# Kernel tuning notes

Hardware: AMD Instinct MI355X
Metric: run time of the kernel (lower is better)

## Reference

```python
import jax, jax.numpy as jnp
import numpy as np

K = 20  # neighbors
EPS = 1e-5

def lrelu(x):
    return jnp.where(x >= 0, x, 0.2 * x)

def knn_idx(x, k):
    # x: [B, C, N] -> idx [B, N, k] of nearest neighbors (includes self)
    xx = jnp.sum(x * x, axis=1)                      # [B, N]
    inner = jnp.einsum('bcn,bcm->bnm', x, x)         # [B, N, N]
    neg_dist = 2.0 * inner - xx[:, :, None] - xx[:, None, :]
    return jax.lax.top_k(neg_dist, k)[1]

def get_graph_feature(x, k):
    # x: [B, C, N] -> [B, 2C, N, k] = concat(neighbor - center, center)
    idx = knn_idx(x, k)                              # [B, N, k]
    xt = jnp.transpose(x, (0, 2, 1))                 # [B, N, C]
    nb = jax.vmap(lambda t, i: t[i])(xt, idx)        # [B, N, k, C]
    ctr = jnp.broadcast_to(xt[:, :, None, :], nb.shape)
    feat = jnp.concatenate([nb - ctr, ctr], axis=-1) # [B, N, k, 2C]
    return jnp.transpose(feat, (0, 3, 1, 2))

def conv_bn2d(x, W, g, b):
    # 1x1 Conv2d (no bias) + training-mode BN + LeakyReLU(0.2)
    y = jnp.einsum('oc,bcnk->bonk', W, x)
    m = jnp.mean(y, axis=(0, 2, 3), keepdims=True)
    v = jnp.var(y, axis=(0, 2, 3), keepdims=True)
    y = g.reshape(1, -1, 1, 1) * (y - m) * jax.lax.rsqrt(v + EPS) + b.reshape(1, -1, 1, 1)
    return lrelu(y)

def conv_bn1d(x, W, g, b):
    y = jnp.einsum('oc,bcn->bon', W, x)
    m = jnp.mean(y, axis=(0, 2), keepdims=True)
    v = jnp.var(y, axis=(0, 2), keepdims=True)
    y = g.reshape(1, -1, 1) * (y - m) * jax.lax.rsqrt(v + EPS) + b.reshape(1, -1, 1)
    return lrelu(y)

def bn_vec(y, g, b):
    m = jnp.mean(y, axis=0, keepdims=True)
    v = jnp.var(y, axis=0, keepdims=True)
    return g * (y - m) * jax.lax.rsqrt(v + EPS) + b

def setup_inputs() -> dict:
    key = jax.random.key(0)
    ks = jax.random.split(key, 16)
    s = 0.05
    d = {
        'x':  jax.random.normal(ks[0], (8, 3, 1024), dtype=jnp.float32),
        'W1': jax.random.normal(ks[1], (64, 6)) * s,
        'W2': jax.random.normal(ks[2], (64, 128)) * s,
        'W3': jax.random.normal(ks[3], (128, 128)) * s,
        'W4': jax.random.normal(ks[4], (256, 256)) * s,
        'W5': jax.random.normal(ks[5], (1024, 512)) * s,
        'Wl1': jax.random.normal(ks[6], (512, 2048)) * s,
        'Wl2': jax.random.normal(ks[7], (256, 512)) * s,
        'bl2': jnp.zeros((256,)),
        'Wl3': jax.random.normal(ks[8], (40, 256)) * s,
        'bl3': jnp.zeros((40,)),
    }
    for i, c in zip(range(1, 8), [64, 64, 128, 256, 1024, 512, 256]):
        d[f'g{i}'] = 1.0 + s * jax.random.normal(jax.random.fold_in(key, 100 + i), (c,))
        d[f'b{i}'] = s * jax.random.normal(jax.random.fold_in(key, 200 + i), (c,))
    return d

def reference(x, W1, W2, W3, W4, W5, Wl1, Wl2, bl2, Wl3, bl3,
              g1, b1, g2, b2, g3, b3, g4, b4, g5, b5, g6, b6, g7, b7):
    f = get_graph_feature(x, K)          # [B, 6, N, k]
    x1 = conv_bn2d(f, W1, g1, b1).max(axis=-1)   # [B, 64, N]
    f = get_graph_feature(x1, K)
    x2 = conv_bn2d(f, W2, g2, b2).max(axis=-1)   # [B, 64, N]
    f = get_graph_feature(x2, K)
    x3 = conv_bn2d(f, W3, g3, b3).max(axis=-1)   # [B, 128, N]
    f = get_graph_feature(x3, K)
    x4 = conv_bn2d(f, W4, g4, b4).max(axis=-1)   # [B, 256, N]
    h = jnp.concatenate([x1, x2, x3, x4], axis=1)  # [B, 512, N]
    h = conv_bn1d(h, W5, g5, b5)                   # [B, 1024, N]
    z = jnp.concatenate([h.max(axis=-1), h.mean(axis=-1)], axis=1)  # [B, 2048]
    z = lrelu(bn_vec(z @ Wl1.T, g6, b6))
    z = lrelu(bn_vec(z @ Wl2.T + bl2, g7, b7))
    return z @ Wl3.T + bl3
```

## Files before the change

kernel.cpp:

```cpp
#include <hip/hip_runtime.h>
#include <hip/hip_bf16.h>
#include <cstdint>


static constexpr int BB  = 8;
static constexpr int NN  = 1024;
static constexpr int KNB = 20;
static constexpr float BNEPS = 1e-5f;

static constexpr int NIN = 25;

__constant__ int c_cum[NIN + 1] = {
    0, 24576, 24960, 33152, 49536, 115072, 639360,
    1687936, 1819008, 1819264, 1829504, 1829544, 1829608, 1829672, 1829736,
    1829800, 1829928, 1830056, 1830312, 1830568, 1831592, 1832616, 1833128,
    1833640, 1833896, 1834152};
__constant__ int c_trO[NIN] = {0, 64, 64, 128, 256, 1024, 0, 0, 0, 0, 0,
                               0, 0, 0, 0, 0, 0, 0, 0, 0, 0, 0, 0, 0, 0};
__constant__ int c_trI[NIN] = {0, 6, 128, 128, 256, 512, 0, 0, 0, 0, 0,
                               0, 0, 0, 0, 0, 0, 0, 0, 0, 0, 0, 0, 0, 0};

enum : int {
  XIN = 0, WT1 = 24576, WT2 = 24960, WT3 = 33152, WT4 = 49536, WT5 = 115072,
  WL1 = 639360, WL2 = 1687936, BL2o = 1819008, WL3 = 1819264, BL3o = 1829504,
  G1 = 1829544, B1o = 1829608, G2 = 1829672, B2o = 1829736,
  G3 = 1829800, B3o = 1829928, G4 = 1830056, B4o = 1830312,
  G5 = 1830568, B5o = 1831592, G6 = 1832616, B6o = 1833128,
  G7 = 1833640, B7o = 1833896,
  IDXo = 1842432,
  HCATo = 2006272,
  STATSo = 6200576,
  Z2048o = 6237440,
  Z1o = 6253824,
  Z2o = 6257920,
  FLAGSo = 6259968,
  DISTo = 6260736,
  HBFo  = 14649344,
  W5BFo = 16746496
};
static constexpr int TOTAL_IN = 1834152;
static constexpr int NCONV = (TOTAL_IN + 255) / 256;
static constexpr int U_OFF   = DISTo + 0;
static constexpr int VD_OFF  = DISTo + 2097152;
static constexpr int YS_OFF  = DISTo + 4194304;
static constexpr int Y5_OFF  = DISTo + 0;
static constexpr size_t WS_NEED_MFMA = (size_t)17008640 * 4;

struct Ptrs { const void* p[NIN]; };

typedef short short8v __attribute__((ext_vector_type(8)));
typedef float f32x16 __attribute__((ext_vector_type(16)));

__device__ __forceinline__ float lrelu(float y) { return (y < 0.f) ? 0.2f * y : y; }
__device__ __forceinline__ unsigned short f2b(float f) {
  unsigned u = __float_as_uint(f);
  unsigned r = (u + 0x7FFFu + ((u >> 16) & 1u)) >> 16;
  return (unsigned short)r;
}
__device__ __forceinline__ unsigned f2s(float f) {
  const unsigned s = __float_as_uint(f);
  return s ^ ((unsigned)((int)s >> 31) | 0x80000000u);
}
__device__ __forceinline__ bool kbetter_u(unsigned v, int i, unsigned v2, int i2) {
  return v > v2 || (v == v2 && i < i2);
}
__device__ __forceinline__ float load_in(const void* p, int fl, int idx) {
  if (fl == 2) return 0.f;
  if (fl == 1) {
    const unsigned short u = ((const unsigned short*)p)[idx];
    return __uint_as_float(((unsigned)u) << 16);
  }
  return ((const float*)p)[idx];
}
__device__ __forceinline__ int mbcnt64(unsigned long long m) {
  return __builtin_amdgcn_mbcnt_hi((unsigned)(m >> 32),
                                   __builtin_amdgcn_mbcnt_lo((unsigned)m, 0));
}

__global__ void detect_kernel(Ptrs ptrs, int* __restrict__ flags) {
  const int i = blockIdx.x;
  const unsigned* p = (const unsigned*)ptrs.p[i];
  const int n = c_cum[i + 1] - c_cum[i];
  int words = n >> 1; if (words > 64) words = 64;
  const int t = threadIdx.x;
  unsigned w = (t < words) ? p[t] : 0u;
  bool nz = (w != 0u);
  unsigned e = (w >> 7) & 0xFFu;
  bool pl = nz && (e >= 96u) && (e <= 140u);
  unsigned long long mnz = __ballot(nz);
  unsigned long long mpl = __ballot(pl);
  if (t == 0) {
    int cnz = __popcll(mnz), cpl = __popcll(mpl);
    flags[i] = (cnz == 0) ? 2 : ((2 * cpl > words) ? 1 : 0);
  }
}

__global__ void convert_kernel(Ptrs ptrs, const int* __restrict__ flags,
                               float* __restrict__ ws, int do_w5) {
  const int bx = blockIdx.x;
  const int t = threadIdx.x;
  if (bx >= NCONV + 80) {
    if (!do_w5) return;
    const int g = (bx - NCONV - 80) * 256 + t;
    const int lane = g & 63;
    const int kb = (g >> 6) & 31;
    const int ot = g >> 11;
    const int o = ot * 32 + (lane & 31);
    const int k0 = kb * 16 + (lane >> 5) * 8;
    const void* w5raw = ptrs.p[5];
    const int fl = flags[5];
    unsigned u[4];
#pragma unroll
    for (int h = 0; h < 4; ++h) {
      const unsigned short lo = f2b(load_in(w5raw, fl, o * 512 + k0 + 2 * h));
      const unsigned short hi = f2b(load_in(w5raw, fl, o * 512 + k0 + 2 * h + 1));
      u[h] = (unsigned)lo | ((unsigned)hi << 16);
    }
    unsigned short* w5p = (unsigned short*)(ws + W5BFo);
    *(uint4*)&w5p[(size_t)g * 8] = make_uint4(u[0], u[1], u[2], u[3]);
    return;
  }
  if (bx >= NCONV) {
    const int z = (bx - NCONV) * 256 + t;
    if (z < 20480) ws[STATSo + z] = 0.f;
    return;
  }
  const int e = bx * 256 + t;
  if (e >= TOTAL_IN) return;
  int i = 0;
  while (e >= c_cum[i + 1]) ++i;
  if (do_w5 && i == 5) return;
  const int el = e - c_cum[i];
  int src;
  const int O = c_trO[i];
  if (O > 0) {
    const int I = c_trI[i];
    const int o = el % O, ii = el / O;
    src = o * I + ii;
  } else src = el;
  ws[e] = load_in(ptrs.p[i], flags[i], src);
}

template <int C>
__global__ __launch_bounds__(256) void dist2_kernel(
    const float* __restrict__ xbase, int bstr, float* __restrict__ D) {
  __shared__ __align__(16) float s_a[16][128];
  __shared__ __align__(16) float s_b[16][128];
  __shared__ float s_xx[256];
  const int t = threadIdx.x;
  const int bx = blockIdx.x;
  const int b = bx >> 6;
  const int r = bx & 63;
  const int tn0 = (r >> 3) * 128;
  const int tm0 = (r & 7) * 128;
  const float* xb = xbase + (size_t)b * bstr;
  {
    const int idx = (t < 128) ? (tn0 + t) : (tm0 + (t - 128));
    float s = 0.f;
    for (int c = 0; c < C; ++c) {
      const float v = xb[c * NN + idx];
      s = fmaf(v, v, s);
    }
    s_xx[t] = s;
  }
  const int tn = (t >> 4) * 8;
  const int tm = (t & 15) * 8;
  float acc[8][8] = {};
  for (int c0 = 0; c0 < C; c0 += 16) {
    const int kc = (C - c0 < 16) ? (C - c0) : 16;
    __syncthreads();
    for (int i = t; i < 512; i += 256) {
      const int cc = i >> 5, col4 = (i & 31) * 4;
      float4 va = make_float4(0.f, 0.f, 0.f, 0.f), vb = va;
      if (cc < kc) {
        va = *(const float4*)&xb[(c0 + cc) * NN + tn0 + col4];
        vb = *(const float4*)&xb[(c0 + cc) * NN + tm0 + col4];
      }
      *(float4*)&s_a[cc][col4] = va;
      *(float4*)&s_b[cc][col4] = vb;
    }
    __syncthreads();
#pragma unroll
    for (int cc = 0; cc < 16; ++cc) {
      const float4 a0 = *(const float4*)&s_a[cc][tn];
      const float4 a1 = *(const float4*)&s_a[cc][tn + 4];
      const float4 b0 = *(const float4*)&s_b[cc][tm];
      const float4 b1 = *(const float4*)&s_b[cc][tm + 4];
      const float aa[8] = {a0.x, a0.y, a0.z, a0.w, a1.x, a1.y, a1.z, a1.w};
      const float bb2[8] = {b0.x, b0.y, b0.z, b0.w, b1.x, b1.y, b1.z, b1.w};
#pragma unroll
      for (int i = 0; i < 8; ++i)
#pragma unroll
        for (int j = 0; j < 8; ++j) acc[i][j] = fmaf(aa[i], bb2[j], acc[i][j]);
    }
  }
  float xmv[8];
#pragma unroll
  for (int j = 0; j < 8; ++j) xmv[j] = s_xx[128 + tm + j];
  float* Db = D + ((size_t)b << 20);
#pragma unroll
  for (int i = 0; i < 8; ++i) {
    const float xxn = s_xx[tn + i];
    float4 o0v, o1v;
    o0v.x = 2.f * acc[i][0] - xxn - xmv[0];
    o0v.y = 2.f * acc[i][1] - xxn - xmv[1];
    o0v.z = 2.f * acc[i][2] - xxn - xmv[2];
    o0v.w = 2.f * acc[i][3] - xxn - xmv[3];
    o1v.x = 2.f * acc[i][4] - xxn - xmv[4];
    o1v.y = 2.f * acc[i][5] - xxn - xmv[5];
    o1v.z = 2.f * acc[i][6] - xxn - xmv[6];
    o1v.w = 2.f * acc[i][7] - xxn - xmv[7];
    float* row = &Db[(size_t)(tn0 + tn + i) * NN + tm0 + tm];
    *(float4*)row = o0v;
    *(float4*)(row + 4) = o1v;
  }
}

__device__ __forceinline__ void tk_ins_u(unsigned v, int i, unsigned ku[4],
                                         int ki[4]) {
  if (kbetter_u(v, i, ku[3], ki[3])) {
    ku[3] = v; ki[3] = i;
    if (kbetter_u(ku[3], ki[3], ku[2], ki[2])) {
      unsigned tv = ku[2]; int ti = ki[2];
      ku[2] = ku[3]; ki[2] = ki[3]; ku[3] = tv; ki[3] = ti;
    }
    if (kbetter_u(ku[2], ki[2], ku[1], ki[1])) {
      unsigned tv = ku[1]; int ti = ki[1];
      ku[1] = ku[2]; ki[1] = ki[2]; ku[2] = tv; ki[2] = ti;
    }
    if (kbetter_u(ku[1], ki[1], ku[0], ki[0])) {
      unsigned tv = ku[0]; int ti = ki[0];
      ku[0] = ku[1]; ki[0] = ki[1]; ku[1] = tv; ki[1] = ti;
    }
  }
}

__device__ __forceinline__ void tk_build_u(const float* __restrict__ Dr,
                                           int base, unsigned mask,
                                           unsigned ku[4], int ki[4]) {
#pragma unroll
  for (int q = 0; q < 4; ++q) { ku[q] = 0u; ki[q] = 0x7FFFFFFF; }
  const float4 a0 = *(const float4*)&Dr[base + 0];
  const float4 a1 = *(const float4*)&Dr[base + 4];
  const float4 a2 = *(const float4*)&Dr[base + 8];
  const float4 a3 = *(const float4*)&Dr[base + 12];
  const float vs[16] = {a0.x, a0.y, a0.z, a0.w, a1.x, a1.y, a1.z, a1.w,
                        a2.x, a2.y, a2.z, a2.w, a3.x, a3.y, a3.z, a3.w};
#pragma unroll
  for (int j = 0; j < 16; ++j)
    if (!((mask >> j) & 1u)) tk_ins_u(f2s(vs[j]), base + j, ku, ki);
}

template <int C, int O>
__global__ __launch_bounds__(256) void tg_kernel(
    const float* __restrict__ D, int* __restrict__ idxb,
    const float* __restrict__ xbase, int bstr, const float* __restrict__ WT,
    float* __restrict__ U, float* __restrict__ Vd) {
  constexpr int OT = O / 64;
  __shared__ __align__(16) float s_pool[1536];
  const int t = threadIdx.x;
  if (blockIdx.x < 2048) {
    const int lane = t & 63;
    const int wv = t >> 6;
    const int row = blockIdx.x * 4 + wv;
    const float* Dr = D + ((size_t)row << 10);
    const int base = lane * 16;
    const float4 a0 = *(const float4*)&Dr[base + 0];
    const float4 a1 = *(const float4*)&Dr[base + 4];
    const float4 a2 = *(const float4*)&Dr[base + 8];
    const float4 a3 = *(const float4*)&Dr[base + 12];
    unsigned k[16] = {f2s(a0.x), f2s(a0.y), f2s(a0.z), f2s(a0.w),
                      f2s(a1.x), f2s(a1.y), f2s(a1.z), f2s(a1.w),
                      f2s(a2.x), f2s(a2.y), f2s(a2.z), f2s(a2.w),
                      f2s(a3.x), f2s(a3.y), f2s(a3.z), f2s(a3.w)};
    unsigned lmax = 0u;
#pragma unroll
    for (int j = 0; j < 16; ++j) lmax = (k[j] > lmax) ? k[j] : lmax;
    unsigned T = 0u;
    for (int b = 31; b >= 0; --b) {
      const unsigned cand = T | (1u << b);
      if (__popcll(__ballot(lmax >= cand)) >= KNB) T = cand;
    }
    int cnt = 0;
#pragma unroll
    for (int j = 0; j < 16; ++j) cnt += (k[j] >= T) ? 1 : 0;
    int n_c = 0, off = 0;
#pragma unroll
    for (int b = 0; b < 5; ++b) {
      const unsigned long long m = __ballot((cnt >> b) & 1);
      n_c += __popcll(m) << b;
      off += mbcnt64(m) << b;
    }
    unsigned long long* sc = (unsigned long long*)s_pool + wv * 128;
    if (n_c <= 128) {
#pragma unroll
      for (int j = 0; j < 16; ++j)
        if (k[j] >= T) {
          sc[off] = (((unsigned long long)k[j]) << 32) |
                    (unsigned long long)(0xFFFFFFFFu ^ (unsigned)(base + j));
          ++off;
        }
      if (n_c <= 64) {
        unsigned long long mye = 0ULL;
        if (lane < n_c) mye = sc[lane];
        int rank = 0;
        for (int j = 0; j < n_c; ++j) {
          const unsigned eh =
              (unsigned)__builtin_amdgcn_readlane((int)(mye >> 32), j);
          const unsigned el =
              (unsigned)__builtin_amdgcn_readlane((int)(mye & 0xFFFFFFFFu), j);
          const unsigned long long ej = (((unsigned long long)eh) << 32) | el;
          rank += (ej > mye) ? 1 : 0;
        }
        if (lane < n_c && rank < KNB)
          idxb[row * KNB + rank] =
              (int)(0xFFFFFFFFu ^ (unsigned)(mye & 0xFFFFFFFFu));
      } else {
        const unsigned long long mye = (lane < n_c) ? sc[lane] : 0ULL;
        const unsigned long long mye2 = (64 + lane < n_c) ? sc[64 + lane] : 0ULL;
        int r1 = 0, r2 = 0;
        for (int j = 0; j < n_c; ++j) {
          const unsigned long long ej = sc[j];
          r1 += (ej > mye) ? 1 : 0;
          r2 += (ej > mye2) ? 1 : 0;
        }
        if (lane < n_c && r1 < KNB)
          idxb[row * KNB + r1] = (int)(0xFFFFFFFFu ^ (unsigned)mye);
        if (64 + lane < n_c && r2 < KNB)
          idxb[row * KNB + r2] = (int)(0xFFFFFFFFu ^ (unsigned)mye2);
      }
      return;
    }
    unsigned ku[4]; int ki[4];
    tk_build_u(Dr, base, 0u, ku, ki);
    unsigned maskex = 0;
    for (int kk = 0; kk < KNB; ++kk) {
      unsigned bv = ku[0];
#pragma unroll
      for (int off2 = 1; off2 < 64; off2 <<= 1) {
        const unsigned pv = (unsigned)__shfl_xor((int)bv, off2, 64);
        bv = (pv > bv) ? pv : bv;
      }
      const unsigned long long m = __ballot(ku[0] == bv);
      const int wl = __ffsll(m) - 1;
      const int bi = __shfl(ki[0], wl, 64);
      if (lane == 0) idxb[row * KNB + kk] = bi;
      if (lane == wl) {
        maskex |= 1u << (bi & 15);
        ku[0] = ku[1]; ki[0] = ki[1];
        ku[1] = ku[2]; ki[1] = ki[2];
        ku[2] = ku[3]; ki[2] = ki[3];
        ku[3] = 0u; ki[3] = 0x7FFFFFFF;
        if (ki[0] == 0x7FFFFFFF && __popc(maskex) < 16)
          tk_build_u(Dr, base, maskex, ku, ki);
      }
    }
    return;
  }
  float (*s_x)[64] = (float(*)[64])(s_pool);
  float (*s_wn)[64] = (float(*)[64])(s_pool + 512);
  float (*s_wc)[64] = (float(*)[64])(s_pool + 1024);
  const int bx = blockIdx.x - 2048;
  const int b = bx / (16 * OT);
  const int r = bx % (16 * OT);
  const int n0 = (r / OT) * 64;
  const int o0 = (r % OT) * 64;
  const float* xb = xbase + (size_t)b * bstr;
  const int tn = (t >> 4) * 4;
  const int to = (t & 15) * 4;
  float accU[4][4] = {}, accC[4][4] = {};
  for (int c0 = 0; c0 < C; c0 += 8) {
    const int kc = (C - c0 < 8) ? (C - c0) : 8;
    for (int i = t; i < 8 * 64; i += 256) {
      const int cc = i >> 6, col = i & 63;
      const bool ok = cc < kc;
      s_x[cc][col]  = ok ? xb[(c0 + cc) * NN + n0 + col] : 0.f;
      s_wn[cc][col] = ok ? WT[(c0 + cc) * O + o0 + col] : 0.f;
      s_wc[cc][col] = ok ? WT[(C + c0 + cc) * O + o0 + col] : 0.f;
    }
    __syncthreads();
#pragma unroll
    for (int cc = 0; cc < 8; ++cc) {
      const float4 xv = *(const float4*)&s_x[cc][tn];
      const float4 wn = *(const float4*)&s_wn[cc][to];
      const float4 wc = *(const float4*)&s_wc[cc][to];
      const float xa[4] = {xv.x, xv.y, xv.z, xv.w};
      const float na[4] = {wn.x, wn.y, wn.z, wn.w};
      const float ca[4] = {wc.x, wc.y, wc.z, wc.w};
#pragma unroll
      for (int i = 0; i < 4; ++i)
#pragma unroll
        for (int j = 0; j < 4; ++j) {
          accU[i][j] = fmaf(xa[i], na[j], accU[i][j]);
          accC[i][j] = fmaf(xa[i], ca[j], accC[i][j]);
        }
    }
    __syncthreads();
  }
#pragma unroll
  for (int i = 0; i < 4; ++i) {
    const size_t base2 = ((size_t)(b << 10) + n0 + tn + i) * O + o0 + to;
    *(float4*)&U[base2] = make_float4(accU[i][0], accU[i][1], accU[i][2], accU[i][3]);
    *(float4*)&Vd[base2] = make_float4(accC[i][0] - accU[i][0], accC[i][1] - accU[i][1],
                                       accC[i][2] - accU[i][2], accC[i][3] - accU[i][3]);
  }
}

template <int O>
__global__ __launch_bounds__(256) void edge_pass_kernel(
    const float* __restrict__ U, const float* __restrict__ Vd,
    const int* __restrict__ idxb, const float* __restrict__ g,
    float* __restrict__ stats, float* __restrict__ ysel) {
  constexpr int PSUB = 256 / O;
  __shared__ float s_red[256];
  const int t = threadIdx.x;
  const int o = t & (O - 1);
  const int psub = t / O;
  const bool usemax = g[o] >= 0.f;
  float ls1 = 0.f, ls2 = 0.f;
  for (int p = blockIdx.x * PSUB + psub; p < BB * NN; p += gridDim.x * PSUB) {
    const int b = p >> 10;
    const float* ub = U + ((size_t)(b << 10)) * O;
    int id[KNB];
#pragma unroll
    for (int k = 0; k < KNB; ++k) id[k] = idxb[p * KNB + k];
    const float vd = Vd[(size_t)p * O + o];
    float ymx = -3.4e38f, ymn = 3.4e38f;
#pragma unroll
    for (int k = 0; k < KNB; ++k) {
      const float y = ub[(size_t)id[k] * O + o] + vd;
      ymx = fmaxf(ymx, y);
      ymn = fminf(ymn, y);
      ls1 += y;
      ls2 = fmaf(y, y, ls2);
    }
    ysel[(size_t)p * O + o] = usemax ? ymx : ymn;
  }
  if (PSUB == 1) {
    atomicAdd(&stats[o], ls1);
    atomicAdd(&stats[1024 + o], ls2);
  } else {
    s_red[t] = ls1;
    __syncthreads();
    if (t < O) {
      float s = s_red[t];
#pragma unroll
      for (int p2 = 1; p2 < PSUB; ++p2) s += s_red[t + p2 * O];
      atomicAdd(&stats[t], s);
    }
    __syncthreads();
    s_red[t] = ls2;
    __syncthreads();
    if (t < O) {
      float s = s_red[t];
#pragma unroll
      for (int p2 = 1; p2 < PSUB; ++p2) s += s_red[t + p2 * O];
      atomicAdd(&stats[1024 + t], s);
    }
  }
}

template <int O>
__global__ __launch_bounds__(256) void bn_apply_kernel(
    const float* __restrict__ ysel, const float* __restrict__ stats,
    const float* __restrict__ g, const float* __restrict__ bb,
    float* __restrict__ hout, unsigned short* __restrict__ hp, int coff) {
  constexpr int OT = O / 32;
  __shared__ float s_t[32][33];
  const int t = threadIdx.x;
  const int bx = blockIdx.x;
  const int b = bx / (32 * OT);
  const int r = bx % (32 * OT);
  const int n0 = (r / OT) * 32;
  const int o0 = (r % OT) * 32;
  const int col = t & 31, rowb = t >> 5;
  const int o = o0 + col;
  const float inv = 1.f / (8.f * 1024.f * 20.f);
  const float mean = stats[o] * inv;
  const float var = stats[1024 + o] * inv - mean * mean;
  const float sc = g[o] * rsqrtf(var + BNEPS);
  const float sh = bb[o] - mean * sc;
  const int c = coff + o;
#pragma unroll
  for (int rr = 0; rr < 4; ++rr) {
    const int nl = n0 + rowb + rr * 8;
    const float y = ysel[((size_t)(b << 10) + nl) * O + o];
    const float h = lrelu(fmaf(sc, y, sh));
    if (hout) s_t[rowb + rr * 8][col] = h;
    if (hp) {
      const int lane2 = (nl & 31) + ((c >> 3) & 1) * 32;
      hp[(((size_t)(b * 32 + (nl >> 5)) * 32 + (c >> 4)) * 64 + lane2) * 8 +
         (c & 7)] = f2b(h);
    }
  }
  if (hout) {
    __syncthreads();
#pragma unroll
    for (int rr = 0; rr < 4; ++rr) {
      const int ol = rowb + rr * 8;
      hout[(size_t)b * (512 * 1024) + (o0 + ol) * NN + n0 + col] = s_t[col][ol];
    }
  }
}

__global__ __launch_bounds__(256) void conv1d_mfma_kernel(
    const unsigned short* __restrict__ hp,
    const unsigned short* __restrict__ w5p, float* __restrict__ Y5) {
  const int t = threadIdx.x, bx = blockIdx.x;
  const int b = bx >> 6;
  const int r = bx & 63;
  const int w = t >> 6, lane = t & 63;
  const int ot0 = (r >> 3) * 4 + (w & 1) * 2;
  const int nt0 = (r & 7) * 4 + (w >> 1) * 2;
  const unsigned short* a0p = w5p + (size_t)ot0 * 16384 + lane * 8;
  const unsigned short* a1p = a0p + 16384;
  const unsigned short* b0p = hp + (size_t)(b * 32 + nt0) * 16384 + lane * 8;
  const unsigned short* b1p = b0p + 16384;
  f32x16 acc00, acc01, acc10, acc11;
#pragma unroll
  for (int i = 0; i < 16; ++i) { acc00[i] = 0.f; acc01[i] = 0.f; acc10[i] = 0.f; acc11[i] = 0.f; }
#pragma unroll 2
  for (int kb = 0; kb < 32; ++kb) {
    const int off = kb * 512;
    const short8v a0 = *(const short8v*)(a0p + off);
    const short8v a1 = *(const short8v*)(a1p + off);
    const short8v b0 = *(const short8v*)(b0p + off);
    const short8v b1 = *(const short8v*)(b1p + off);
    acc00 = __builtin_amdgcn_mfma_f32_32x32x16_bf16(a0, b0, acc00, 0, 0, 0);
    acc01 = __builtin_amdgcn_mfma_f32_32x32x16_bf16(a0, b1, acc01, 0, 0, 0);
    acc10 = __builtin_amdgcn_mfma_f32_32x32x16_bf16(a1, b0, acc10, 0, 0, 0);
    acc11 = __builtin_amdgcn_mfma_f32_32x32x16_bf16(a1, b1, acc11, 0, 0, 0);
  }
  const int l31 = lane & 31, l5 = lane >> 5;
#pragma unroll
  for (int oi = 0; oi < 2; ++oi) {
#pragma unroll
    for (int nj = 0; nj < 2; ++nj) {
      const f32x16 a = (oi == 0) ? (nj == 0 ? acc00 : acc01)
                                 : (nj == 0 ? acc10 : acc11);
      const int ob = (ot0 + oi) * 32;
      const int nb = (nt0 + nj) * 32;
#pragma unroll
      for (int r16 = 0; r16 < 16; ++r16) {
        const int row = (r16 & 3) + 8 * (r16 >> 2) + 4 * l5;
        Y5[((size_t)(b << 10) + ob + row) * 1024 + nb + l31] = a[r16];
      }
    }
  }
}

__global__ __launch_bounds__(256) void c1pool_kernel(
    const float* __restrict__ Y5, const float* __restrict__ g,
    const float* __restrict__ bb, float* __restrict__ z) {
  __shared__ __align__(16) float s_y[8][1024];
  __shared__ float sr[256];
  __shared__ float s_par[2];
  const int o = blockIdx.x, t = threadIdx.x;
  float s1 = 0.f, s2 = 0.f;
#pragma unroll
  for (int b = 0; b < 8; ++b) {
    const float4 v = *(const float4*)&Y5[((size_t)((b << 10) + o)) * 1024 + t * 4];
    *(float4*)&s_y[b][t * 4] = v;
    s1 += v.x + v.y + v.z + v.w;
    s2 = fmaf(v.x, v.x, s2);
    s2 = fmaf(v.y, v.y, s2);
    s2 = fmaf(v.z, v.z, s2);
    s2 = fmaf(v.w, v.w, s2);
  }
  sr[t] = s1;
  __syncthreads();
  for (int s = 128; s > 0; s >>= 1) {
    if (t < s) sr[t] += sr[t + s];
    __syncthreads();
  }
  if (t == 0) s_par[0] = sr[0];
  __syncthreads();
  sr[t] = s2;
  __syncthreads();
  for (int s = 128; s > 0; s >>= 1) {
    if (t < s) sr[t] += sr[t + s];
    __syncthreads();
  }
  if (t == 0) {
    const float mean = s_par[0] * (1.f / 8192.f);
    const float var = sr[0] * (1.f / 8192.f) - mean * mean;
    const float sc = g[o] * rsqrtf(var + BNEPS);
    s_par[0] = sc;
    s_par[1] = bb[o] - mean * sc;
  }
  __syncthreads();
  const float sc = s_par[0], sh = s_par[1];
  const int lane = t & 63, w = t >> 6;
#pragma unroll
  for (int h = 0; h < 2; ++h) {
    const int b = w + h * 4;
    float mx = -3.4e38f, sm = 0.f;
#pragma unroll
    for (int j = 0; j < 4; ++j) {
      const float4 v = *(const float4*)&s_y[b][lane * 16 + j * 4];
      const float y0 = lrelu(fmaf(sc, v.x, sh));
      const float y1 = lrelu(fmaf(sc, v.y, sh));
      const float y2 = lrelu(fmaf(sc, v.z, sh));
      const float y3 = lrelu(fmaf(sc, v.w, sh));
      mx = fmaxf(fmaxf(fmaxf(mx, y0), fmaxf(y1, y2)), y3);
      sm += y0 + y1 + y2 + y3;
    }
#pragma unroll
    for (int off = 1; off < 64; off <<= 1) {
      mx = fmaxf(mx, __shfl_xor(mx, off, 64));
      sm += __shfl_xor(sm, off, 64);
    }
    if (lane == 0) {
      z[b * 2048 + o] = mx;
      z[b * 2048 + 1024 + o] = sm * (1.f / 1024.f);
    }
  }
}

__global__ void bn_finalize_kernel(float* __restrict__ stats,
                                   const float* __restrict__ g,
                                   const float* __restrict__ bb, int cout,
                                   float inv_cnt) {
  const int o = blockIdx.x * 256 + threadIdx.x;
  if (o >= cout) return;
  const float mean = stats[o] * inv_cnt;
  const float var = stats[1024 + o] * inv_cnt - mean * mean;
  const float s = g[o] * rsqrtf(var + BNEPS);
  stats[2048 + o] = s;
  stats[3072 + o] = bb[o] - mean * s;
}

__global__ __launch_bounds__(256) void conv1d_gemm_kernel(
    const float* __restrict__ hcat, const float* __restrict__ WT5,
    float* __restrict__ stats, float* __restrict__ Y5) {
  __shared__ __align__(16) float s_w[8][64];
  __shared__ __align__(16) float s_h[8][64];
  __shared__ __align__(16) float s_red[64][16];
  const int t = threadIdx.x;
  const int bx = blockIdx.x;
  const int b = bx >> 8;
  const int o0 = ((bx >> 4) & 15) * 64;
  const int n0 = (bx & 15) * 64;
  const float* hb = hcat + (size_t)b * (512 * 1024);
  const int to = (t >> 4) * 4;
  const int tn = (t & 15) * 4;
  float acc[4][4] = {};
  for (int c0 = 0; c0 < 512; c0 += 8) {
    for (int i = t; i < 8 * 64; i += 256) {
      const int cc = i >> 6, col = i & 63;
      s_w[cc][col] = WT5[(c0 + cc) * 1024 + o0 + col];
      s_h[cc][col] = hb[(c0 + cc) * NN + n0 + col];
    }
    __syncthreads();
#pragma unroll
    for (int cc = 0; cc < 8; ++cc) {
      const float4 wv = *(const float4*)&s_w[cc][to];
      const float4 hv = *(const float4*)&s_h[cc][tn];
      const float wa[4] = {wv.x, wv.y, wv.z, wv.w};
      const float ha[4] = {hv.x, hv.y, hv.z, hv.w};
#pragma unroll
      for (int i = 0; i < 4; ++i)
#pragma unroll
        for (int j = 0; j < 4; ++j) acc[i][j] = fmaf(wa[i], ha[j], acc[i][j]);
    }
    __syncthreads();
  }
#pragma unroll
  for (int i = 0; i < 4; ++i) {
    *(float4*)&Y5[((size_t)(b << 10) + o0 + to + i) * NN + n0 + tn] =
        make_float4(acc[i][0], acc[i][1], acc[i][2], acc[i][3]);
  }
#pragma unroll
  for (int i = 0; i < 4; ++i)
    s_red[to + i][t & 15] = acc[i][0] + acc[i][1] + acc[i][2] + acc[i][3];
  __syncthreads();
  if (t < 64) {
    float s = 0.f;
#pragma unroll
    for (int g2 = 0; g2 < 16; ++g2) s += s_red[t][g2];
    atomicAdd(&stats[o0 + t], s);
  }
  __syncthreads();
#pragma unroll
  for (int i = 0; i < 4; ++i) {
    float s = 0.f;
#pragma unroll
    for (int j = 0; j < 4; ++j) s = fmaf(acc[i][j], acc[i][j], s);
    s_red[to + i][t & 15] = s;
  }
  __syncthreads();
  if (t < 64) {
    float s = 0.f;
#pragma unroll
    for (int g2 = 0; g2 < 16; ++g2) s += s_red[t][g2];
    atomicAdd(&stats[1024 + o0 + t], s);
  }
}

__global__ __launch_bounds__(256) void pool_kernel(
    const float* __restrict__ Y5, const float* __restrict__ stats,
    float* __restrict__ z) {
  const int t = threadIdx.x;
  const int lane = t & 63;
  const int bx = blockIdx.x;
  const int b = bx >> 8;
  const int o = (bx & 255) * 4 + (t >> 6);
  const float sc = stats[2048 + o], sh = stats[3072 + o];
  const float* yr = Y5 + ((size_t)(b << 10) + o) * NN;
  float mx = -3.4e38f, sm = 0.f;
#pragma unroll
  for (int j = 0; j < 16; ++j) {
    const float y = lrelu(fmaf(sc, yr[j * 64 + lane], sh));
    mx = fmaxf(mx, y);
    sm += y;
  }
  for (int off = 32; off > 0; off >>= 1) {
    mx = fmaxf(mx, __shfl_down(mx, off, 64));
    sm += __shfl_down(sm, off, 64);
  }
  if (lane == 0) {
    z[b * 2048 + o] = mx;
    z[b * 2048 + 1024 + o] = sm * (1.f / 1024.f);
  }
}

__global__ __launch_bounds__(256) void mlp_kernel(
    const float* __restrict__ zin, const float* __restrict__ W,
    const float* __restrict__ bias, const float* __restrict__ g,
    const float* __restrict__ bb, int kin, float* __restrict__ out, int O) {
  __shared__ float s_red[256];
  __shared__ float s_y[8];
  const int t = threadIdx.x;
  const int o = blockIdx.x;
  float acc[8];
#pragma unroll
  for (int b = 0; b < 8; ++b) acc[b] = 0.f;
  for (int c = t; c < kin; c += 256) {
    const float w = W[(size_t)o * kin + c];
#pragma unroll
    for (int b = 0; b < 8; ++b) acc[b] = fmaf(w, zin[b * kin + c], acc[b]);
  }
  for (int b = 0; b < 8; ++b) {
    s_red[t] = acc[b];
    __syncthreads();
    for (int s = 128; s > 0; s >>= 1) {
      if (t < s) s_red[t] += s_red[t + s];
      __syncthreads();
    }
    if (t == 0) s_y[b] = s_red[0] + (bias ? bias[o] : 0.f);
    __syncthreads();
  }
  if (t == 0) {
    float m = 0.f;
    for (int b = 0; b < 8; ++b) m += s_y[b];
    m *= 0.125f;
    float v = 0.f;
    for (int b = 0; b < 8; ++b) { const float d = s_y[b] - m; v = fmaf(d, d, v); }
    v *= 0.125f;
    const float s = g[o] * rsqrtf(v + BNEPS);
    const float sh = bb[o] - m * s;
    for (int b = 0; b < 8; ++b) out[b * O + o] = lrelu(fmaf(s, s_y[b], sh));
  }
}

__global__ void final_kernel(const float* __restrict__ z2,
                             const float* __restrict__ Wl3,
                             const float* __restrict__ bl3,
                             const int* __restrict__ flags, void* out) {
  const int j = blockIdx.x * 256 + threadIdx.x;
  if (j >= 320) return;
  int anyf32 = 0, anybf = 0;
  for (int i = 0; i < NIN; ++i) {
    const int fl = flags[i];
    if (fl == 0) anyf32 = 1;
    if (fl == 1) anybf = 1;
  }
  const int bf16out = (anybf && !anyf32) ? 1 : 0;
  const int b = j / 40, o = j - b * 40;
  float s = bl3[o];
  for (int c = 0; c < 256; ++c) s = fmaf(z2[b * 256 + c], Wl3[o * 256 + c], s);
  if (bf16out) ((__hip_bfloat16*)out)[j] = __float2bfloat16(s);
  else ((float*)out)[j] = s;
}

template <int C, int O>
static void run_stage(float* wsf, const float* xbase, int bstr, int widx,
                      int gidx, int bidx, int stat, float* hout,
                      unsigned short* hp, int coff, hipStream_t stream) {
  int* idxb = reinterpret_cast<int*>(wsf + IDXo);
  float* dist = wsf + DISTo;
  float* U = wsf + U_OFF;
  float* Vd = wsf + VD_OFF;
  float* ysel = wsf + YS_OFF;
  float* stats = wsf + STATSo + stat * 4096;
  dist2_kernel<C><<<512, 256, 0, stream>>>(xbase, bstr, dist);
  tg_kernel<C, O><<<2048 + BB * 16 * (O / 64), 256, 0, stream>>>(
      dist, idxb, xbase, bstr, wsf + widx, U, Vd);
  edge_pass_kernel<O><<<512, 256, 0, stream>>>(U, Vd, idxb, wsf + gidx, stats,
                                               ysel);
  bn_apply_kernel<O><<<BB * 32 * (O / 32), 256, 0, stream>>>(
      ysel, stats, wsf + gidx, wsf + bidx, hout, hp, coff);
}

extern "C" void kernel_launch(void* const* d_in, const int* in_sizes, int n_in,
                              void* d_out, int out_size, void* d_ws,
                              size_t ws_size, hipStream_t stream) {
  (void)in_sizes; (void)n_in; (void)out_size;
  float* wsf = reinterpret_cast<float*>(d_ws);
  int* flags = reinterpret_cast<int*>(wsf + FLAGSo);
  float* hcat = wsf + HCATo;
  const bool mf = ws_size >= WS_NEED_MFMA;
  unsigned short* hp = mf ? reinterpret_cast<unsigned short*>(wsf + HBFo) : nullptr;
  unsigned short* w5p = reinterpret_cast<unsigned short*>(wsf + W5BFo);

  Ptrs ptrs;
  for (int i = 0; i < NIN; ++i) ptrs.p[i] = d_in[i];

  detect_kernel<<<NIN, 64, 0, stream>>>(ptrs, flags);
  convert_kernel<<<NCONV + 80 + 256, 256, 0, stream>>>(ptrs, flags, wsf,
                                                       mf ? 1 : 0);

  run_stage<3, 64>(wsf, wsf + XIN, 3 * NN, WT1, G1, B1o, 0, hcat, hp, 0,
                   stream);
  run_stage<64, 64>(wsf, hcat, 512 * NN, WT2, G2, B2o, 1, hcat + 64 * NN, hp,
                    64, stream);
  run_stage<64, 128>(wsf, hcat + 64 * NN, 512 * NN, WT3, G3, B3o, 2,
                     hcat + 128 * NN, hp, 128, stream);
  run_stage<128, 256>(wsf, hcat + 128 * NN, 512 * NN, WT4, G4, B4o, 3,
                      mf ? nullptr : (hcat + 256 * NN), hp, 256, stream);

  float* Y5 = wsf + Y5_OFF;
  float* st5 = wsf + STATSo + 4 * 4096;
  if (mf) {
    conv1d_mfma_kernel<<<512, 256, 0, stream>>>(hp, w5p, Y5);
    c1pool_kernel<<<1024, 256, 0, stream>>>(Y5, wsf + G5, wsf + B5o,
                                            wsf + Z2048o);
  } else {
    conv1d_gemm_kernel<<<2048, 256, 0, stream>>>(hcat, wsf + WT5, st5, Y5);
    bn_finalize_kernel<<<4, 256, 0, stream>>>(st5, wsf + G5, wsf + B5o, 1024,
                                              1.f / 8192.f);
    pool_kernel<<<BB * 256, 256, 0, stream>>>(Y5, st5, wsf + Z2048o);
  }

  mlp_kernel<<<512, 256, 0, stream>>>(wsf + Z2048o, wsf + WL1, nullptr,
      wsf + G6, wsf + B6o, 2048, wsf + Z1o, 512);
  mlp_kernel<<<256, 256, 0, stream>>>(wsf + Z1o, wsf + WL2, wsf + BL2o,
      wsf + G7, wsf + B7o, 512, wsf + Z2o, 256);
  final_kernel<<<2, 256, 0, stream>>>(wsf + Z2o, wsf + WL3, wsf + BL3o,
      flags, d_out);
}
```

Measured before the change: 470.5 us.

## Skip converting MLP weights; read raw inputs directly in MLP kernels

When the MFMA path is active, the convert kernel now only processes the small leading inputs and the BN parameter tail, skipping the large Wl1/Wl2/Wl3 copies into workspace. The MLP and final kernels instead read the original input buffers through the dtype-aware loader using the detected flags. The edge_pass kernel grid is also raised from 512 to 2048 blocks to add parallelism. The direct reads add a per-element flag branch in the MLP loops. The larger edge_pass grid assumes the kernel handles the extra blocks correctly.

```diff
diff --git a/kernel.cpp b/kernel.cpp
--- a/kernel.cpp
+++ b/kernel.cpp
@@ -40,6 +40,8 @@
 };
 static constexpr int TOTAL_IN = 1834152;
 static constexpr int NCONV = (TOTAL_IN + 255) / 256;
+static constexpr int NMAIN_ELEMS = 115072 + 4608;
+static constexpr int NMAIN_MF = (NMAIN_ELEMS + 255) / 256;
 static constexpr int U_OFF   = DISTo + 0;
 static constexpr int VD_OFF  = DISTo + 2097152;
 static constexpr int YS_OFF  = DISTo + 4194304;
@@ -96,12 +98,12 @@
 }
 
 __global__ void convert_kernel(Ptrs ptrs, const int* __restrict__ flags,
-                               float* __restrict__ ws, int do_w5) {
+                               float* __restrict__ ws, int do_w5, int nmain) {
   const int bx = blockIdx.x;
   const int t = threadIdx.x;
-  if (bx >= NCONV + 80) {
+  if (bx >= nmain + 80) {
     if (!do_w5) return;
-    const int g = (bx - NCONV - 80) * 256 + t;
+    const int g = (bx - nmain - 80) * 256 + t;
     const int lane = g & 63;
     const int kb = (g >> 6) & 31;
     const int ot = g >> 11;
@@ -120,16 +122,22 @@
     *(uint4*)&w5p[(size_t)g * 8] = make_uint4(u[0], u[1], u[2], u[3]);
     return;
   }
-  if (bx >= NCONV) {
-    const int z = (bx - NCONV) * 256 + t;
+  if (bx >= nmain) {
+    const int z = (bx - nmain) * 256 + t;
     if (z < 20480) ws[STATSo + z] = 0.f;
     return;
   }
-  const int e = bx * 256 + t;
-  if (e >= TOTAL_IN) return;
+  int e;
+  if (do_w5) {
+    const int e2 = bx * 256 + t;
+    if (e2 >= NMAIN_ELEMS) return;
+    e = (e2 < 115072) ? e2 : (e2 - 115072 + 1829544);
+  } else {
+    e = bx * 256 + t;
+    if (e >= TOTAL_IN) return;
+  }
   int i = 0;
   while (e >= c_cum[i + 1]) ++i;
-  if (do_w5 && i == 5) return;
   const int el = e - c_cum[i];
   int src;
   const int O = c_trO[i];
@@ -725,18 +733,20 @@
 }
 
 __global__ __launch_bounds__(256) void mlp_kernel(
-    const float* __restrict__ zin, const float* __restrict__ W,
-    const float* __restrict__ bias, const float* __restrict__ g,
-    const float* __restrict__ bb, int kin, float* __restrict__ out, int O) {
+    const float* __restrict__ zin, const void* __restrict__ W,
+    const void* __restrict__ bias, const int* __restrict__ flags, int wfl,
+    int bfl, const float* __restrict__ g, const float* __restrict__ bb,
+    int kin, float* __restrict__ out, int O) {
   __shared__ float s_red[256];
   __shared__ float s_y[8];
   const int t = threadIdx.x;
   const int o = blockIdx.x;
+  const int fw = flags[wfl];
   float acc[8];
 #pragma unroll
   for (int b = 0; b < 8; ++b) acc[b] = 0.f;
   for (int c = t; c < kin; c += 256) {
-    const float w = W[(size_t)o * kin + c];
+    const float w = load_in(W, fw, o * kin + c);
 #pragma unroll
     for (int b = 0; b < 8; ++b) acc[b] = fmaf(w, zin[b * kin + c], acc[b]);
   }
@@ -747,7 +757,8 @@
       if (t < s) s_red[t] += s_red[t + s];
       __syncthreads();
     }
-    if (t == 0) s_y[b] = s_red[0] + (bias ? bias[o] : 0.f);
+    if (t == 0)
+      s_y[b] = s_red[0] + (bias ? load_in(bias, flags[bfl], o) : 0.f);
     __syncthreads();
   }
   if (t == 0) {
@@ -764,8 +775,8 @@
 }
 
 __global__ void final_kernel(const float* __restrict__ z2,
-                             const float* __restrict__ Wl3,
-                             const float* __restrict__ bl3,
+                             const void* __restrict__ Wl3,
+                             const void* __restrict__ bl3,
                              const int* __restrict__ flags, void* out) {
   const int j = blockIdx.x * 256 + threadIdx.x;
   if (j >= 320) return;
@@ -776,9 +787,11 @@
     if (fl == 1) anybf = 1;
   }
   const int bf16out = (anybf && !anyf32) ? 1 : 0;
+  const int fw = flags[9], fb = flags[10];
   const int b = j / 40, o = j - b * 40;
-  float s = bl3[o];
-  for (int c = 0; c < 256; ++c) s = fmaf(z2[b * 256 + c], Wl3[o * 256 + c], s);
+  float s = load_in(bl3, fb, o);
+  for (int c = 0; c < 256; ++c)
+    s = fmaf(z2[b * 256 + c], load_in(Wl3, fw, o * 256 + c), s);
   if (bf16out) ((__hip_bfloat16*)out)[j] = __float2bfloat16(s);
   else ((float*)out)[j] = s;
 }
@@ -796,8 +809,8 @@
   dist2_kernel<C><<<512, 256, 0, stream>>>(xbase, bstr, dist);
   tg_kernel<C, O><<<2048 + BB * 16 * (O / 64), 256, 0, stream>>>(
       dist, idxb, xbase, bstr, wsf + widx, U, Vd);
-  edge_pass_kernel<O><<<512, 256, 0, stream>>>(U, Vd, idxb, wsf + gidx, stats,
-                                               ysel);
+  edge_pass_kernel<O><<<2048, 256, 0, stream>>>(U, Vd, idxb, wsf + gidx,
+                                                stats, ysel);
   bn_apply_kernel<O><<<BB * 32 * (O / 32), 256, 0, stream>>>(
       ysel, stats, wsf + gidx, wsf + bidx, hout, hp, coff);
 }
@@ -817,8 +830,9 @@
   for (int i = 0; i < NIN; ++i) ptrs.p[i] = d_in[i];
 
   detect_kernel<<<NIN, 64, 0, stream>>>(ptrs, flags);
-  convert_kernel<<<NCONV + 80 + 256, 256, 0, stream>>>(ptrs, flags, wsf,
-                                                       mf ? 1 : 0);
+  const int nmain = mf ? NMAIN_MF : NCONV;
+  convert_kernel<<<nmain + 80 + 256, 256, 0, stream>>>(ptrs, flags, wsf,
+                                                       mf ? 1 : 0, nmain);
 
   run_stage<3, 64>(wsf, wsf + XIN, 3 * NN, WT1, G1, B1o, 0, hcat, hp, 0,
                    stream);
@@ -842,10 +856,10 @@
     pool_kernel<<<BB * 256, 256, 0, stream>>>(Y5, st5, wsf + Z2048o);
   }
 
-  mlp_kernel<<<512, 256, 0, stream>>>(wsf + Z2048o, wsf + WL1, nullptr,
-      wsf + G6, wsf + B6o, 2048, wsf + Z1o, 512);
-  mlp_kernel<<<256, 256, 0, stream>>>(wsf + Z1o, wsf + WL2, wsf + BL2o,
-      wsf + G7, wsf + B7o, 512, wsf + Z2o, 256);
-  final_kernel<<<2, 256, 0, stream>>>(wsf + Z2o, wsf + WL3, wsf + BL3o,
+  mlp_kernel<<<512, 256, 0, stream>>>(wsf + Z2048o, d_in[6], nullptr, flags,
+      6, 0, wsf + G6, wsf + B6o, 2048, wsf + Z1o, 512);
+  mlp_kernel<<<256, 256, 0, stream>>>(wsf + Z1o, d_in[7], d_in[8], flags,
+      7, 8, wsf + G7, wsf + B7o, 512, wsf + Z2o, 256);
+  final_kernel<<<2, 256, 0, stream>>>(wsf + Z2o, d_in[9], d_in[10],
       flags, d_out);
 }
```

Result: slower. 606.5 us (+28.9%).
